# Performance work log

Hardware: AMD Instinct MI355X
Metric: run time of the kernel (lower is better)

Reference implementation:

```python
import jax, jax.numpy as jnp
import numpy as np

NUM_USERS = 200000
NUM_ITEMS = 100000
D = 128
NNZ = 2000000
L = 2  # opt['GNN']


def spmm(rows, cols, vals, x, n_out):
    # sparse [n_out, n_in] @ dense [n_in, d] via gather + segment_sum
    return jax.ops.segment_sum(vals[:, None] * x[cols], rows, num_segments=n_out)


def setup_inputs() -> dict:
    key = jax.random.key(0)
    ks = jax.random.split(key, 12)
    return {
        "ufea": jax.random.normal(ks[0], (NUM_USERS, D), jnp.float32),
        "vfea": jax.random.normal(ks[1], (NUM_ITEMS, D), jnp.float32),
        "uv_rows": jax.random.randint(ks[2], (NNZ,), 0, NUM_USERS, jnp.int32),
        "uv_cols": jax.random.randint(ks[3], (NNZ,), 0, NUM_ITEMS, jnp.int32),
        "uv_vals": jax.random.uniform(ks[4], (NNZ,), jnp.float32),
        "vu_rows": jax.random.randint(ks[5], (NNZ,), 0, NUM_ITEMS, jnp.int32),
        "vu_cols": jax.random.randint(ks[6], (NNZ,), 0, NUM_USERS, jnp.int32),
        "vu_vals": jax.random.uniform(ks[7], (NNZ,), jnp.float32),
        "user_W": jax.random.normal(ks[8], (L, 2 * D, D), jnp.float32) * 0.05,
        "user_b": jax.random.normal(ks[9], (L, D), jnp.float32) * 0.05,
        "item_W": jax.random.normal(ks[10], (L, 2 * D, D), jnp.float32) * 0.05,
        "item_b": jax.random.normal(ks[11], (L, D), jnp.float32) * 0.05,
    }


def reference(ufea, vfea, uv_rows, uv_cols, uv_vals,
              vu_rows, vu_cols, vu_vals,
              user_W, user_b, item_W, item_b):
    learn_user, learn_item = ufea, vfea
    for l in range(L):
        # dropout is identity at inference (training=False)
        # two-hop aggregation through the bipartite graph
        user_ho = spmm(vu_rows, vu_cols, vu_vals, learn_user, NUM_ITEMS)   # [I, D]
        item_ho = spmm(uv_rows, uv_cols, uv_vals, learn_item, NUM_USERS)   # [U, D]
        user_ho = spmm(uv_rows, uv_cols, uv_vals, user_ho, NUM_USERS)      # [U, D]
        item_ho = spmm(vu_rows, vu_cols, vu_vals, item_ho, NUM_ITEMS)      # [I, D]
        user_cat = jnp.concatenate([user_ho, learn_user], axis=1)          # [U, 2D]
        item_cat = jnp.concatenate([item_ho, learn_item], axis=1)          # [I, 2D]
        learn_user = jax.nn.relu(user_cat @ user_W[l] + user_b[l])
        learn_item = jax.nn.relu(item_cat @ item_W[l] + item_b[l])
    return learn_user, learn_item
```

## Files before the change

kernel.cpp:

```cpp
#include <hip/hip_runtime.h>

#define DIM 128
#define N_USERS 200000
#define N_ITEMS 100000
#define CAP_U 40
#define CAP_I 56
#define SCAT_BLOCKS 2048
#define CONV_BLOCKS 512
#define TRANS_BLOCKS 128

typedef __attribute__((ext_vector_type(8))) _Float16 half8;
typedef __attribute__((ext_vector_type(4))) _Float16 half4v;
typedef __attribute__((ext_vector_type(4))) float f32x4;

__device__ __forceinline__ void scatter_body(
    const int* __restrict__ rowsA, const int* __restrict__ colsA,
    const float* __restrict__ valsA, int* __restrict__ degA,
    int2* __restrict__ ellA, int capA, int nA, int rloA, int rhiA,
    const int* __restrict__ rowsB, const int* __restrict__ colsB,
    const float* __restrict__ valsB, int* __restrict__ degB,
    int2* __restrict__ ellB, int capB, int nB, int rloB, int rhiB,
    int t0, int stride)
{
    int nA4 = nA >> 2;
    for (int q = t0; q < nA4; q += stride) {
        int4   r = reinterpret_cast<const int4*>(rowsA)[q];
        int4   c = reinterpret_cast<const int4*>(colsA)[q];
        float4 v = reinterpret_cast<const float4*>(valsA)[q];
        if (r.x >= rloA && r.x < rhiA) { int s = atomicAdd(&degA[r.x], 1); if (s < capA) ellA[(size_t)r.x * capA + s] = make_int2(c.x, __float_as_int(v.x)); }
        if (r.y >= rloA && r.y < rhiA) { int s = atomicAdd(&degA[r.y], 1); if (s < capA) ellA[(size_t)r.y * capA + s] = make_int2(c.y, __float_as_int(v.y)); }
        if (r.z >= rloA && r.z < rhiA) { int s = atomicAdd(&degA[r.z], 1); if (s < capA) ellA[(size_t)r.z * capA + s] = make_int2(c.z, __float_as_int(v.z)); }
        if (r.w >= rloA && r.w < rhiA) { int s = atomicAdd(&degA[r.w], 1); if (s < capA) ellA[(size_t)r.w * capA + s] = make_int2(c.w, __float_as_int(v.w)); }
    }
    for (int t = (nA4 << 2) + t0; t < nA; t += stride) {
        int r = rowsA[t];
        if (r >= rloA && r < rhiA) {
            int s = atomicAdd(&degA[r], 1);
            if (s < capA) ellA[(size_t)r * capA + s] = make_int2(colsA[t], __float_as_int(valsA[t]));
        }
    }
    int nB4 = nB >> 2;
    for (int q = t0; q < nB4; q += stride) {
        int4   r = reinterpret_cast<const int4*>(rowsB)[q];
        int4   c = reinterpret_cast<const int4*>(colsB)[q];
        float4 v = reinterpret_cast<const float4*>(valsB)[q];
        if (r.x >= rloB && r.x < rhiB) { int s = atomicAdd(&degB[r.x], 1); if (s < capB) ellB[(size_t)r.x * capB + s] = make_int2(c.x, __float_as_int(v.x)); }
        if (r.y >= rloB && r.y < rhiB) { int s = atomicAdd(&degB[r.y], 1); if (s < capB) ellB[(size_t)r.y * capB + s] = make_int2(c.y, __float_as_int(v.y)); }
        if (r.z >= rloB && r.z < rhiB) { int s = atomicAdd(&degB[r.z], 1); if (s < capB) ellB[(size_t)r.z * capB + s] = make_int2(c.z, __float_as_int(v.z)); }
        if (r.w >= rloB && r.w < rhiB) { int s = atomicAdd(&degB[r.w], 1); if (s < capB) ellB[(size_t)r.w * capB + s] = make_int2(c.w, __float_as_int(v.w)); }
    }
    for (int t = (nB4 << 2) + t0; t < nB; t += stride) {
        int r = rowsB[t];
        if (r >= rloB && r < rhiB) {
            int s = atomicAdd(&degB[r], 1);
            if (s < capB) ellB[(size_t)r * capB + s] = make_int2(colsB[t], __float_as_int(valsB[t]));
        }
    }
}

__global__ __launch_bounds__(256) void scatter_conv_kernel(
    const int* rowsA, const int* colsA, const float* valsA, int* degA,
    int2* ellA, int capA, int nA, int rloA, int rhiA,
    const int* rowsB, const int* colsB, const float* valsB, int* degB,
    int2* ellB, int capB, int nB, int rloB, int rhiB,
    const float* __restrict__ srcU, _Float16* __restrict__ dstU, int n8U,
    const float* __restrict__ srcV, _Float16* __restrict__ dstV, int n8V)
{
    if ((int)blockIdx.x < SCAT_BLOCKS) {
        scatter_body(rowsA, colsA, valsA, degA, ellA, capA, nA, rloA, rhiA,
                     rowsB, colsB, valsB, degB, ellB, capB, nB, rloB, rhiB,
                     blockIdx.x * 256 + threadIdx.x, SCAT_BLOCKS * 256);
        return;
    }
    int t0 = (blockIdx.x - SCAT_BLOCKS) * 256 + threadIdx.x;
    int stride = CONV_BLOCKS * 256;
    int total = n8U + n8V;
    for (int t = t0; t < total; t += stride) {
        const float* src; _Float16* dst; int i;
        if (t < n8U) { src = srcU; dst = dstU; i = t; }
        else         { src = srcV; dst = dstV; i = t - n8U; }
        const float4* s = reinterpret_cast<const float4*>(src) + (size_t)i * 2;
        float4 a = s[0], b = s[1];
        half8 h;
        h[0] = (_Float16)a.x; h[1] = (_Float16)a.y;
        h[2] = (_Float16)a.z; h[3] = (_Float16)a.w;
        h[4] = (_Float16)b.x; h[5] = (_Float16)b.y;
        h[6] = (_Float16)b.z; h[7] = (_Float16)b.w;
        reinterpret_cast<half8*>(dst)[i] = h;
    }
}

__global__ __launch_bounds__(256) void scatter_trans_kernel(
    const int* rowsA, const int* colsA, const float* valsA, int* degA,
    int2* ellA, int capA, int nA, int rloA, int rhiA,
    const int* rowsB, const int* colsB, const float* valsB, int* degB,
    int2* ellB, int capB, int nB, int rloB, int rhiB,
    const float* __restrict__ Wu, _Float16* __restrict__ Wtu,
    const float* __restrict__ Wi, _Float16* __restrict__ Wti)
{
    if ((int)blockIdx.x < SCAT_BLOCKS) {
        scatter_body(rowsA, colsA, valsA, degA, ellA, capA, nA, rloA, rhiA,
                     rowsB, colsB, valsB, degB, ellB, capB, nB, rloB, rhiB,
                     blockIdx.x * 256 + threadIdx.x, SCAT_BLOCKS * 256);
        return;
    }
    int t0 = (blockIdx.x - SCAT_BLOCKS) * 256 + threadIdx.x;
    int stride = TRANS_BLOCKS * 256;
    for (int t = t0; t < 131072; t += stride) {
        const float* W; _Float16* Wt; int i;
        if (t < 65536) { W = Wu; Wt = Wtu; i = t; }
        else           { W = Wi; Wt = Wti; i = t - 65536; }
        int l = i >> 15;
        int r = i & 32767;
        int k = r >> 7;
        int n = r & 127;
        Wt[(size_t)l * 32768 + n * 256 + k] = (_Float16)W[i];
    }
}

__global__ __launch_bounds__(256) void scatter_plain_kernel(
    const int* rowsA, const int* colsA, const float* valsA, int* degA,
    int2* ellA, int capA, int nA, int rloA, int rhiA,
    const int* rowsB, const int* colsB, const float* valsB, int* degB,
    int2* ellB, int capB, int nB, int rloB, int rhiB)
{
    scatter_body(rowsA, colsA, valsA, degA, ellA, capA, nA, rloA, rhiA,
                 rowsB, colsB, valsB, degB, ellB, capB, nB, rloB, rhiB,
                 blockIdx.x * 256 + threadIdx.x, gridDim.x * 256);
}

__global__ __launch_bounds__(256) void scan1_dual_kernel(
    const int* __restrict__ degU, int* __restrict__ offU, int* __restrict__ bsU,
    int nU, int nbU, int capU,
    const int* __restrict__ degI, int* __restrict__ offI, int* __restrict__ bsI,
    int nI, int nbI, int capI)
{
    __shared__ int lds[256];
    const int* deg; int* out; int* bs; int n, blk, cap;
    if ((int)blockIdx.x < nbU) { deg = degU; out = offU; bs = bsU; n = nU; blk = blockIdx.x; cap = capU; }
    else { deg = degI; out = offI; bs = bsI; n = nI; blk = blockIdx.x - nbU; cap = capI; }

    int tid  = threadIdx.x;
    int base = blk * 1024 + tid * 4;
    int v0 = (base + 0 < n) ? min(deg[base + 0], cap) : 0;
    int v1 = (base + 1 < n) ? min(deg[base + 1], cap) : 0;
    int v2 = (base + 2 < n) ? min(deg[base + 2], cap) : 0;
    int v3 = (base + 3 < n) ? min(deg[base + 3], cap) : 0;
    int s1 = v0 + v1, s2 = s1 + v2, s3 = s2 + v3;
    lds[tid] = s3;
    __syncthreads();
    for (int d = 1; d < 256; d <<= 1) {
        int t = 0;
        if (tid >= d) t = lds[tid - d];
        __syncthreads();
        lds[tid] += t;
        __syncthreads();
    }
    int excl = (tid > 0) ? lds[tid - 1] : 0;
    if (base + 0 < n) out[base + 1] = excl + v0;
    if (base + 1 < n) out[base + 2] = excl + s1;
    if (base + 2 < n) out[base + 3] = excl + s2;
    if (base + 3 < n) out[base + 4] = excl + s3;
    if (tid == 255) bs[blk] = lds[255];
    if (blk == 0 && tid == 0) out[0] = 0;
}

__global__ __launch_bounds__(256) void scan2_dual_kernel(
    int* __restrict__ bsU, int nbU, int* __restrict__ bsI, int nbI)
{
    __shared__ int part[256];
    int* a = (blockIdx.x == 0) ? bsU : bsI;
    int n  = (blockIdx.x == 0) ? nbU : nbI;
    int tid = threadIdx.x;
    int v = (tid < n) ? a[tid] : 0;
    part[tid] = v;
    __syncthreads();
    for (int d = 1; d < 256; d <<= 1) {
        int t = 0;
        if (tid >= d) t = part[tid - d];
        __syncthreads();
        part[tid] += t;
        __syncthreads();
    }
    if (tid < n) a[tid] = (tid > 0) ? part[tid - 1] : 0;
}

__global__ __launch_bounds__(256) void scan3_dual_kernel(
    int* __restrict__ offU, const int* __restrict__ bsU, int nU, int nbU,
    int* __restrict__ offI, const int* __restrict__ bsI, int nI, int nbI)
{
    int* out; const int* bs; int n, blk;
    if ((int)blockIdx.x < nbU) { out = offU; bs = bsU; n = nU; blk = blockIdx.x; }
    else { out = offI; bs = bsI; n = nI; blk = blockIdx.x - nbU; }
    int add  = bs[blk];
    if (add == 0) return;
    int base = blk * 1024 + threadIdx.x * 4;
    if (base + 0 < n) out[base + 1] += add;
    if (base + 1 < n) out[base + 2] += add;
    if (base + 2 < n) out[base + 3] += add;
    if (base + 3 < n) out[base + 4] += add;
}

__global__ __launch_bounds__(256) void pack_dual_kernel(
    const int* __restrict__ degU, const int* __restrict__ offU,
    const int2* __restrict__ ellU, int2* __restrict__ csrU, int nU,
    const int* __restrict__ degI, const int* __restrict__ offI,
    const int2* __restrict__ ellI, int2* __restrict__ csrI, int nI)
{
    int t = blockIdx.x * blockDim.x + threadIdx.x;
    int g = t >> 2, lane = t & 3;
    const int2* src; int2* dst; int d;
    if (g < nU) {
        d = min(degU[g], CAP_U);
        src = ellU + (size_t)g * CAP_U;
        dst = csrU + offU[g];
    } else {
        g -= nU;
        if (g >= nI) return;
        d = min(degI[g], CAP_I);
        src = ellI + (size_t)g * CAP_I;
        dst = csrI + offI[g];
    }
    for (int s = lane; s < d; s += 4) dst[s] = src[s];
}

__global__ __launch_bounds__(256) void spmm_dual_kernel(
    const int* __restrict__ offA, const int2* __restrict__ edgA,
    const _Float16* __restrict__ xA, _Float16* __restrict__ outA, int nA,
    const int* __restrict__ offB, const int2* __restrict__ edgB,
    const _Float16* __restrict__ xB, _Float16* __restrict__ outB, int nB)
{
    int t    = blockIdx.x * blockDim.x + threadIdx.x;
    int grp  = t >> 4;
    int lane = t & 15;

    const int*      off;
    const int2*     edg;
    const _Float16* x;
    _Float16*       out;
    int row;
    if (grp < nA) {
        off = offA; edg = edgA; x = xA; out = outA; row = grp;
    } else {
        row = grp - nA;
        if (row >= nB) return;
        off = offB; edg = edgB; x = xB; out = outB;
    }

    int beg = off[row], end = off[row + 1];
    float acc[8] = {0.f, 0.f, 0.f, 0.f, 0.f, 0.f, 0.f, 0.f};
    int k = beg;
    for (; k + 3 < end; k += 4) {
        int2 e[4];
        half8 xv[4];
#pragma unroll
        for (int u = 0; u < 4; ++u) e[u] = edg[k + u];
#pragma unroll
        for (int u = 0; u < 4; ++u)
            xv[u] = *reinterpret_cast<const half8*>(
                x + (size_t)e[u].x * DIM + lane * 8);
#pragma unroll
        for (int u = 0; u < 4; ++u) {
            float v = __int_as_float(e[u].y);
#pragma unroll
            for (int i = 0; i < 8; ++i) acc[i] += v * (float)xv[u][i];
        }
    }
    for (; k < end; ++k) {
        int2 e0 = edg[k];
        half8 x0 = *reinterpret_cast<const half8*>(x + (size_t)e0.x * DIM + lane * 8);
        float v0 = __int_as_float(e0.y);
#pragma unroll
        for (int i = 0; i < 8; ++i) acc[i] += v0 * (float)x0[i];
    }
    half8 o;
#pragma unroll
    for (int i = 0; i < 8; ++i) o[i] = (_Float16)acc[i];
    *reinterpret_cast<half8*>(out + (size_t)row * DIM + lane * 8) = o;
}

template<int OUT_F32>
__global__ __launch_bounds__(256) void gemm_dual_kernel(
    const _Float16* __restrict__ HOu, const _Float16* __restrict__ CURu,
    const _Float16* __restrict__ Wtu, const float* __restrict__ bu,
    float* __restrict__ outFu, _Float16* __restrict__ outHu, int Mu, int ublocks,
    const _Float16* __restrict__ HOi, const _Float16* __restrict__ CURi,
    const _Float16* __restrict__ Wti, const float* __restrict__ bi,
    float* __restrict__ outFi, _Float16* __restrict__ outHi, int Mi)
{
    const int TILES = 8;
    int bid = blockIdx.x;
    const _Float16 *HO, *CUR, *Wt;
    const float* bias;
    float* outF;
    _Float16* outH;
    int M;
    if (bid < ublocks) {
        HO = HOu; CUR = CURu; Wt = Wtu; bias = bu; outF = outFu; outH = outHu; M = Mu;
    } else {
        bid -= ublocks;
        HO = HOi; CUR = CURi; Wt = Wti; bias = bi; outF = outFi; outH = outHi; M = Mi;
    }

    int tid  = threadIdx.x;
    int wave = tid >> 6;
    int l    = tid & 63;
    int m    = l & 15;
    int kg   = l >> 4;

    half8 wfrag[2][8];
    float4 bv[2];
#pragma unroll
    for (int jj = 0; jj < 2; ++jj) {
        int j = wave * 2 + jj;
#pragma unroll
        for (int kk = 0; kk < 8; ++kk)
            wfrag[jj][kk] = *reinterpret_cast<const half8*>(
                Wt + (size_t)(j * 16 + m) * 256 + kk * 32 + kg * 8);
        bv[jj] = *reinterpret_cast<const float4*>(bias + j * 16 + kg * 4);
    }

    int base = bid * (TILES * 16);
#pragma unroll 2
    for (int t = 0; t < TILES; ++t) {
        int row = base + t * 16 + m;
        int rr  = min(row, M - 1);
        half8 afrag[8];
#pragma unroll
        for (int kk = 0; kk < 8; ++kk) {
            const _Float16* src = (kk < 4) ? HO : CUR;
            int k0 = (kk & 3) * 32 + kg * 8;
            afrag[kk] = *reinterpret_cast<const half8*>(src + (size_t)rr * DIM + k0);
        }
#pragma unroll
        for (int jj = 0; jj < 2; ++jj) {
            f32x4 acc = {0.f, 0.f, 0.f, 0.f};
#pragma unroll
            for (int kk = 0; kk < 8; ++kk)
                acc = __builtin_amdgcn_mfma_f32_16x16x32_f16(
                    wfrag[jj][kk], afrag[kk], acc, 0, 0, 0);
            int n0 = (wave * 2 + jj) * 16 + kg * 4;
            float o0 = fmaxf(acc[0] + bv[jj].x, 0.f);
            float o1 = fmaxf(acc[1] + bv[jj].y, 0.f);
            float o2 = fmaxf(acc[2] + bv[jj].z, 0.f);
            float o3 = fmaxf(acc[3] + bv[jj].w, 0.f);
            if (row < M) {
                if (OUT_F32) {
                    float4 st = make_float4(o0, o1, o2, o3);
                    *reinterpret_cast<float4*>(outF + (size_t)row * DIM + n0) = st;
                } else {
                    half4v st;
                    st[0] = (_Float16)o0; st[1] = (_Float16)o1;
                    st[2] = (_Float16)o2; st[3] = (_Float16)o3;
                    *reinterpret_cast<half4v*>(outH + (size_t)row * DIM + n0) = st;
                }
            }
        }
    }
}

extern "C" void kernel_launch(void* const* d_in, const int* in_sizes, int n_in,
                              void* d_out, int out_size, void* d_ws, size_t ws_size,
                              hipStream_t stream) {
    const float* ufea    = (const float*)d_in[0];
    const float* vfea    = (const float*)d_in[1];
    const int*   uv_rows = (const int*)d_in[2];
    const int*   uv_cols = (const int*)d_in[3];
    const float* uv_vals = (const float*)d_in[4];
    const int*   vu_rows = (const int*)d_in[5];
    const int*   vu_cols = (const int*)d_in[6];
    const float* vu_vals = (const float*)d_in[7];
    const float* user_W  = (const float*)d_in[8];
    const float* user_b  = (const float*)d_in[9];
    const float* item_W  = (const float*)d_in[10];
    const float* item_b  = (const float*)d_in[11];

    const int nnz = in_sizes[2];

    float* out_user = (float*)d_out;
    float* out_item = out_user + (size_t)N_USERS * DIM;

    const size_t UD = (size_t)N_USERS * DIM;
    const size_t ID = (size_t)N_ITEMS * DIM;

    char* p = (char*)d_ws;
    auto alloc = [&](size_t bytes) {
        char* q = p;
        p += (bytes + 255) & ~(size_t)255;
        return q;
    };
    _Float16* Uf = (_Float16*)alloc(UD * 2);
    _Float16* Vf = (_Float16*)alloc(ID * 2);
    _Float16* Ua = (_Float16*)alloc(UD * 2);
    _Float16* Ub = (_Float16*)alloc(UD * 2);
    _Float16* Va = (_Float16*)alloc(ID * 2);
    _Float16* Vb = (_Float16*)alloc(ID * 2);
    _Float16* Vc = (_Float16*)alloc(ID * 2);
    _Float16* Wt_user = (_Float16*)alloc((size_t)2 * 128 * 256 * 2);
    _Float16* Wt_item = (_Float16*)alloc((size_t)2 * 128 * 256 * 2);
    int* deg_all = (int*)alloc((size_t)(N_USERS + N_ITEMS) * 4);
    int* uv_deg  = deg_all;
    int* vu_deg  = deg_all + N_USERS;
    int2* uv_ell = (int2*)alloc((size_t)N_USERS * CAP_U * 8);
    int2* vu_ell = (int2*)alloc((size_t)N_ITEMS * CAP_I * 8);
    int* uv_off  = (int*)alloc((size_t)(N_USERS + 1) * 4);
    int* vu_off  = (int*)alloc((size_t)(N_ITEMS + 1) * 4);
    int* bsU     = (int*)alloc(256 * 4);
    int* bsI     = (int*)alloc(256 * 4);

    int2* uv_csr = (int2*)d_out;
    int2* vu_csr = uv_csr + nnz;

    const int nbU = (N_USERS + 1023) / 1024;
    const int nbI = (N_ITEMS + 1023) / 1024;

    {
        hipMemsetAsync(deg_all, 0, (size_t)(N_USERS + N_ITEMS) * 4, stream);
        const int NPASS = 4;
        int wU = (N_USERS + NPASS - 1) / NPASS;
        int wI = (N_ITEMS + NPASS - 1) / NPASS;

        scatter_conv_kernel<<<SCAT_BLOCKS + CONV_BLOCKS, 256, 0, stream>>>(
            uv_rows, uv_cols, uv_vals, uv_deg, uv_ell, CAP_U, nnz, 0, wU,
            vu_rows, vu_cols, vu_vals, vu_deg, vu_ell, CAP_I, nnz, 0, wI,
            ufea, Uf, (int)(UD / 8), vfea, Vf, (int)(ID / 8));
        scatter_trans_kernel<<<SCAT_BLOCKS + TRANS_BLOCKS, 256, 0, stream>>>(
            uv_rows, uv_cols, uv_vals, uv_deg, uv_ell, CAP_U, nnz, wU, 2 * wU,
            vu_rows, vu_cols, vu_vals, vu_deg, vu_ell, CAP_I, nnz, wI, 2 * wI,
            user_W, Wt_user, item_W, Wt_item);
        for (int pass = 2; pass < NPASS; ++pass) {
            scatter_plain_kernel<<<SCAT_BLOCKS, 256, 0, stream>>>(
                uv_rows, uv_cols, uv_vals, uv_deg, uv_ell, CAP_U, nnz,
                pass * wU, min((pass + 1) * wU, N_USERS),
                vu_rows, vu_cols, vu_vals, vu_deg, vu_ell, CAP_I, nnz,
                pass * wI, min((pass + 1) * wI, N_ITEMS));
        }
    }

    scan1_dual_kernel<<<nbU + nbI, 256, 0, stream>>>(
        uv_deg, uv_off, bsU, N_USERS, nbU, CAP_U,
        vu_deg, vu_off, bsI, N_ITEMS, nbI, CAP_I);
    scan2_dual_kernel<<<2, 256, 0, stream>>>(bsU, nbU, bsI, nbI);
    scan3_dual_kernel<<<nbU + nbI, 256, 0, stream>>>(
        uv_off, bsU, N_USERS, nbU, vu_off, bsI, N_ITEMS, nbI);
    {
        int threads = (N_USERS + N_ITEMS) * 4;
        pack_dual_kernel<<<(threads + 255) / 256, 256, 0, stream>>>(
            uv_deg, uv_off, uv_ell, uv_csr, N_USERS,
            vu_deg, vu_off, vu_ell, vu_csr, N_ITEMS);
    }

    auto spmm_pair = [&](const _Float16* xu, _Float16* outI,
                         const _Float16* xv, _Float16* outU) {
        size_t groups = (size_t)N_ITEMS + N_USERS;
        int blocks = (int)((groups * 16 + 255) / 256);
        spmm_dual_kernel<<<blocks, 256, 0, stream>>>(
            vu_off, vu_csr, xu, outI, N_ITEMS,
            uv_off, uv_csr, xv, outU, N_USERS);
    };

    const int UB = (N_USERS + 127) / 128;
    const int IB = (N_ITEMS + 127) / 128;

    spmm_pair(Uf, Va, Vf, Ua);
    spmm_pair(Ua, Vb, Va, Ub);
    gemm_dual_kernel<0><<<UB + IB, 256, 0, stream>>>(
        Ub, Uf, Wt_user, user_b, (float*)nullptr, Ua, N_USERS, UB,
        Vb, Vf, Wt_item, item_b, (float*)nullptr, Va, N_ITEMS);

    spmm_pair(Ua, Vb, Va, Ub);
    spmm_pair(Ub, Vc, Vb, Uf);
    gemm_dual_kernel<1><<<UB + IB, 256, 0, stream>>>(
        Uf, Ua, Wt_user + 32768, user_b + DIM, out_user, (_Float16*)nullptr, N_USERS, UB,
        Vc, Va, Wt_item + 32768, item_b + DIM, out_item, (_Float16*)nullptr, N_ITEMS);
}
```

Before: 1.089 ms.

## Prefetch SpMM edges, widen pack lanes, double GEMM tiles, lazy scatter loads

```diff
diff --git a/kernel.cpp b/kernel.cpp
--- a/kernel.cpp
+++ b/kernel.cpp
@@ -24,13 +24,12 @@
 {
     int nA4 = nA >> 2;
     for (int q = t0; q < nA4; q += stride) {
-        int4   r = reinterpret_cast<const int4*>(rowsA)[q];
-        int4   c = reinterpret_cast<const int4*>(colsA)[q];
-        float4 v = reinterpret_cast<const float4*>(valsA)[q];
-        if (r.x >= rloA && r.x < rhiA) { int s = atomicAdd(&degA[r.x], 1); if (s < capA) ellA[(size_t)r.x * capA + s] = make_int2(c.x, __float_as_int(v.x)); }
-        if (r.y >= rloA && r.y < rhiA) { int s = atomicAdd(&degA[r.y], 1); if (s < capA) ellA[(size_t)r.y * capA + s] = make_int2(c.y, __float_as_int(v.y)); }
-        if (r.z >= rloA && r.z < rhiA) { int s = atomicAdd(&degA[r.z], 1); if (s < capA) ellA[(size_t)r.z * capA + s] = make_int2(c.z, __float_as_int(v.z)); }
-        if (r.w >= rloA && r.w < rhiA) { int s = atomicAdd(&degA[r.w], 1); if (s < capA) ellA[(size_t)r.w * capA + s] = make_int2(c.w, __float_as_int(v.w)); }
+        int4 r = reinterpret_cast<const int4*>(rowsA)[q];
+        int b = q << 2;
+        if (r.x >= rloA && r.x < rhiA) { int s = atomicAdd(&degA[r.x], 1); if (s < capA) ellA[(size_t)r.x * capA + s] = make_int2(colsA[b + 0], __float_as_int(valsA[b + 0])); }
+        if (r.y >= rloA && r.y < rhiA) { int s = atomicAdd(&degA[r.y], 1); if (s < capA) ellA[(size_t)r.y * capA + s] = make_int2(colsA[b + 1], __float_as_int(valsA[b + 1])); }
+        if (r.z >= rloA && r.z < rhiA) { int s = atomicAdd(&degA[r.z], 1); if (s < capA) ellA[(size_t)r.z * capA + s] = make_int2(colsA[b + 2], __float_as_int(valsA[b + 2])); }
+        if (r.w >= rloA && r.w < rhiA) { int s = atomicAdd(&degA[r.w], 1); if (s < capA) ellA[(size_t)r.w * capA + s] = make_int2(colsA[b + 3], __float_as_int(valsA[b + 3])); }
     }
     for (int t = (nA4 << 2) + t0; t < nA; t += stride) {
         int r = rowsA[t];
@@ -41,13 +40,12 @@
     }
     int nB4 = nB >> 2;
     for (int q = t0; q < nB4; q += stride) {
-        int4   r = reinterpret_cast<const int4*>(rowsB)[q];
-        int4   c = reinterpret_cast<const int4*>(colsB)[q];
-        float4 v = reinterpret_cast<const float4*>(valsB)[q];
-        if (r.x >= rloB && r.x < rhiB) { int s = atomicAdd(&degB[r.x], 1); if (s < capB) ellB[(size_t)r.x * capB + s] = make_int2(c.x, __float_as_int(v.x)); }
-        if (r.y >= rloB && r.y < rhiB) { int s = atomicAdd(&degB[r.y], 1); if (s < capB) ellB[(size_t)r.y * capB + s] = make_int2(c.y, __float_as_int(v.y)); }
-        if (r.z >= rloB && r.z < rhiB) { int s = atomicAdd(&degB[r.z], 1); if (s < capB) ellB[(size_t)r.z * capB + s] = make_int2(c.z, __float_as_int(v.z)); }
-        if (r.w >= rloB && r.w < rhiB) { int s = atomicAdd(&degB[r.w], 1); if (s < capB) ellB[(size_t)r.w * capB + s] = make_int2(c.w, __float_as_int(v.w)); }
+        int4 r = reinterpret_cast<const int4*>(rowsB)[q];
+        int b = q << 2;
+        if (r.x >= rloB && r.x < rhiB) { int s = atomicAdd(&degB[r.x], 1); if (s < capB) ellB[(size_t)r.x * capB + s] = make_int2(colsB[b + 0], __float_as_int(valsB[b + 0])); }
+        if (r.y >= rloB && r.y < rhiB) { int s = atomicAdd(&degB[r.y], 1); if (s < capB) ellB[(size_t)r.y * capB + s] = make_int2(colsB[b + 1], __float_as_int(valsB[b + 1])); }
+        if (r.z >= rloB && r.z < rhiB) { int s = atomicAdd(&degB[r.z], 1); if (s < capB) ellB[(size_t)r.z * capB + s] = make_int2(colsB[b + 2], __float_as_int(valsB[b + 2])); }
+        if (r.w >= rloB && r.w < rhiB) { int s = atomicAdd(&degB[r.w], 1); if (s < capB) ellB[(size_t)r.w * capB + s] = make_int2(colsB[b + 3], __float_as_int(valsB[b + 3])); }
     }
     for (int t = (nB4 << 2) + t0; t < nB; t += stride) {
         int r = rowsB[t];
@@ -208,7 +206,7 @@
     const int2* __restrict__ ellI, int2* __restrict__ csrI, int nI)
 {
     int t = blockIdx.x * blockDim.x + threadIdx.x;
-    int g = t >> 2, lane = t & 3;
+    int g = t >> 3, lane = t & 7;
     const int2* src; int2* dst; int d;
     if (g < nU) {
         d = min(degU[g], CAP_U);
@@ -221,7 +219,7 @@
         src = ellI + (size_t)g * CAP_I;
         dst = csrI + offI[g];
     }
-    for (int s = lane; s < d; s += 4) dst[s] = src[s];
+    for (int s = lane; s < d; s += 8) dst[s] = src[s];
 }
 
 __global__ __launch_bounds__(256) void spmm_dual_kernel(
@@ -250,21 +248,32 @@
     int beg = off[row], end = off[row + 1];
     float acc[8] = {0.f, 0.f, 0.f, 0.f, 0.f, 0.f, 0.f, 0.f};
     int k = beg;
-    for (; k + 3 < end; k += 4) {
-        int2 e[4];
+    int2 e[4];
+    if (k + 3 < end) {
+#pragma unroll
+        for (int u = 0; u < 4; ++u) e[u] = edg[k + u];
+    }
+    while (k + 3 < end) {
         half8 xv[4];
-#pragma unroll
-        for (int u = 0; u < 4; ++u) e[u] = edg[k + u];
 #pragma unroll
         for (int u = 0; u < 4; ++u)
             xv[u] = *reinterpret_cast<const half8*>(
                 x + (size_t)e[u].x * DIM + lane * 8);
+        int kn = k + 4;
+        int2 en[4];
+        if (kn + 3 < end) {
+#pragma unroll
+            for (int u = 0; u < 4; ++u) en[u] = edg[kn + u];
+        }
 #pragma unroll
         for (int u = 0; u < 4; ++u) {
             float v = __int_as_float(e[u].y);
 #pragma unroll
             for (int i = 0; i < 8; ++i) acc[i] += v * (float)xv[u][i];
         }
+#pragma unroll
+        for (int u = 0; u < 4; ++u) e[u] = en[u];
+        k = kn;
     }
     for (; k < end; ++k) {
         int2 e0 = edg[k];
@@ -288,7 +297,7 @@
     const _Float16* __restrict__ Wti, const float* __restrict__ bi,
     float* __restrict__ outFi, _Float16* __restrict__ outHi, int Mi)
 {
-    const int TILES = 8;
+    const int TILES = 16;
     int bid = blockIdx.x;
     const _Float16 *HO, *CUR, *Wt;
     const float* bias;
@@ -444,7 +453,7 @@
     scan3_dual_kernel<<<nbU + nbI, 256, 0, stream>>>(
         uv_off, bsU, N_USERS, nbU, vu_off, bsI, N_ITEMS, nbI);
     {
-        int threads = (N_USERS + N_ITEMS) * 4;
+        int threads = (N_USERS + N_ITEMS) * 8;
         pack_dual_kernel<<<(threads + 255) / 256, 256, 0, stream>>>(
             uv_deg, uv_off, uv_ell, uv_csr, N_USERS,
             vu_deg, vu_off, vu_ell, vu_csr, N_ITEMS);
@@ -459,8 +468,8 @@
             uv_off, uv_csr, xv, outU, N_USERS);
     };
 
-    const int UB = (N_USERS + 127) / 128;
-    const int IB = (N_ITEMS + 127) / 128;
+    const int UB = (N_USERS + 255) / 256;
+    const int IB = (N_ITEMS + 255) / 256;
 
     spmm_pair(Uf, Va, Vf, Ua);
     spmm_pair(Ua, Vb, Va, Ub);
```

Measured after the change: 1.061 ms. -2.6%, faster.
